# Kernel optimization log

Measured on AMD Instinct MI355X. Metric: run time of the kernel, lower is better.

The kernel has to match this reference:

```python
import jax, jax.numpy as jnp
import numpy as np

# dims: T timesteps (=window_size[0]), B_ = num_windows*batch, window 8x8, C=dim
T, B, WH, WW, C, NH = 4, 1024, 8, 8, 256, 8
HD = C // NH          # head_dim = 32
N = T * WH * WW       # tokens per window volume = 256
V_TH, TAU, ALPHA = 1.0, 2.0, 4.0  # LIF threshold, membrane tau, surrogate sharpness

@jax.custom_vjp
def spike(v):
    # Heaviside spike with sigmoid surrogate gradient (standard spikingjelly-style)
    return (v >= 0.0).astype(v.dtype)

def _spike_fwd(v):
    return spike(v), v

def _spike_bwd(v, g):
    sg = jax.nn.sigmoid(ALPHA * v)
    return (g * ALPHA * sg * (1.0 - sg),)

spike.defvjp(_spike_fwd, _spike_bwd)

def lif(x):
    """Multi-step LIF neuron over leading time axis. x: (T, ...). Hard reset to 0."""
    def step(v, xt):
        v = v + (xt - v) / TAU
        s = spike(v - V_TH)
        return v * (1.0 - s), s
    _, s = jax.lax.scan(step, jnp.zeros_like(x[0]), x)
    return s

def setup_inputs() -> dict:
    key = jax.random.key(0)
    ks = jax.random.split(key, 6)
    sc = 1.0 / np.sqrt(C)
    return {
        "x":   jax.random.normal(ks[0], (T, B, WH, WW, C), jnp.float32),
        "Wq":  jax.random.normal(ks[1], (C, C), jnp.float32) * sc,   # linear_q weight (no bias)
        "Wk":  jax.random.normal(ks[2], (C, C), jnp.float32) * sc,   # linear_k weight (no bias)
        "Wp":  jax.random.normal(ks[3], (C, C), jnp.float32) * sc,   # proj weight
        "bp":  jnp.zeros((C,), jnp.float32),                         # proj bias
        "pos": jax.random.normal(ks[4], (1, NH, N, HD), jnp.float32) * 0.02,  # positional_encoding param
    }

def reference(x, Wq, Wk, Wp, bp, pos):
    # proj_sn on raw input
    xs = lif(x)                                        # (T,B,WH,WW,C) spikes
    # Q path: linear -> spiking neuron (norm=None branch skipped)
    q = lif(xs @ Wq.T)                                 # (T,B,WH,WW,C)
    # K path: linear -> add positional encoding -> spiking neuron
    k = lif(xs @ Wk.T + pos.reshape(T, 1, WH, WW, C))  # (T,B,WH,WW,C)
    # head split exactly as torch reshapes (row-major, mixes T into B for k)
    q = q.reshape(T, B, NH, WH * WW, HD)
    k = k.reshape(B, NH, T * WH * WW, HD)
    # token attention: sum over head_dim, spike, elementwise multiply with k
    att_token = lif(q.sum(-1, keepdims=True))          # (T,B,NH,HW,1)
    attn = k * att_token.reshape(B, NH, -1, 1)         # (B,NH,T*HW,HD)
    # exact torch permute/reshape back to (T,B,WH,WW,C)
    x2 = attn.reshape(B, NH, T, WH, WW, HD).transpose(2, 0, 3, 4, 1, 5).reshape(T, B, WH, WW, C)
    attn_out = lif(x2)                                 # attn_sn output (second return value)
    y = (x2 @ Wp.T + bp).reshape(B, N, C)              # proj then final reshape (B_, N, C)
    return y, attn_out
```

## Files before the change

### kernel.cpp

```cpp
#include <hip/hip_runtime.h>
#include <hip/hip_bf16.h>

static constexpr int  G     = 65536;
static constexpr long PLANE = 16777216L;

__device__ __forceinline__ float bfh(unsigned short u) {
    union { unsigned u32; float f; } c; c.u32 = ((unsigned)u) << 16; return c.f;
}

__global__ void prep_kernel(const float* __restrict__ Wq, const float* __restrict__ Wk,
                            const float* __restrict__ Wp,
                            __hip_bfloat16* __restrict__ WqT, __hip_bfloat16* __restrict__ WkT,
                            float* __restrict__ WpT, unsigned* __restrict__ flag)
{
    int c = blockIdx.x;
    int j = threadIdx.x;
    int idx = c * 256 + j;
    WqT[idx] = __float2bfloat16(Wq[j * 256 + c]);
    WkT[idx] = __float2bfloat16(Wk[j * 256 + c]);
    WpT[idx] = Wp[j * 256 + c];
    if (c == 0 && j == 0) *flag = 0u;
}

__device__ __forceinline__ void gather_word(unsigned long long mm, int j, int lane,
                                            const __hip_bfloat16* __restrict__ WT,
                                            float& q0, float& q1, float& q2, float& q3)
{
    if (!mm) return;
    int b = __ffsll(mm) - 1; mm &= (mm - 1);
    ushort4 w = *((const ushort4*)(WT + (4 * b + j) * 256 + 4 * lane));
    while (mm) {
        int b2 = __ffsll(mm) - 1; mm &= (mm - 1);
        ushort4 w2 = *((const ushort4*)(WT + (4 * b2 + j) * 256 + 4 * lane));
        q0 += bfh(w.x); q1 += bfh(w.y); q2 += bfh(w.z); q3 += bfh(w.w);
        w = w2;
    }
    q0 += bfh(w.x); q1 += bfh(w.y); q2 += bfh(w.z); q3 += bfh(w.w);
}

__device__ __forceinline__ void gather8(
    unsigned long long m0, unsigned long long m1, unsigned long long m2, unsigned long long m3,
    unsigned long long n0, unsigned long long n1, unsigned long long n2, unsigned long long n3,
    const __hip_bfloat16* __restrict__ WT, int lane,
    float4& qa, float4& qb)
{
    const __hip_bfloat16* base = WT + 4 * lane;
    ushort4 w0 = {0,0,0,0}, w1 = {0,0,0,0}, w2 = {0,0,0,0}, w3 = {0,0,0,0};
    ushort4 x0 = {0,0,0,0}, x1 = {0,0,0,0}, x2 = {0,0,0,0}, x3 = {0,0,0,0};
    while (m0 | m1 | m2 | m3 | n0 | n1 | n2 | n3) {
        bool h0 = m0 != 0, h1 = m1 != 0, h2 = m2 != 0, h3 = m3 != 0;
        bool g0 = n0 != 0, g1 = n1 != 0, g2 = n2 != 0, g3 = n3 != 0;
        if (h0) { int b = __ffsll(m0) - 1; m0 &= m0 - 1; w0 = *(const ushort4*)(base + (4*b+0)*256); }
        if (h1) { int b = __ffsll(m1) - 1; m1 &= m1 - 1; w1 = *(const ushort4*)(base + (4*b+1)*256); }
        if (h2) { int b = __ffsll(m2) - 1; m2 &= m2 - 1; w2 = *(const ushort4*)(base + (4*b+2)*256); }
        if (h3) { int b = __ffsll(m3) - 1; m3 &= m3 - 1; w3 = *(const ushort4*)(base + (4*b+3)*256); }
        if (g0) { int b = __ffsll(n0) - 1; n0 &= n0 - 1; x0 = *(const ushort4*)(base + (4*b+0)*256); }
        if (g1) { int b = __ffsll(n1) - 1; n1 &= n1 - 1; x1 = *(const ushort4*)(base + (4*b+1)*256); }
        if (g2) { int b = __ffsll(n2) - 1; n2 &= n2 - 1; x2 = *(const ushort4*)(base + (4*b+2)*256); }
        if (g3) { int b = __ffsll(n3) - 1; n3 &= n3 - 1; x3 = *(const ushort4*)(base + (4*b+3)*256); }
        if (h0) { qa.x += bfh(w0.x); qa.y += bfh(w0.y); qa.z += bfh(w0.z); qa.w += bfh(w0.w); }
        if (h1) { qa.x += bfh(w1.x); qa.y += bfh(w1.y); qa.z += bfh(w1.z); qa.w += bfh(w1.w); }
        if (h2) { qa.x += bfh(w2.x); qa.y += bfh(w2.y); qa.z += bfh(w2.z); qa.w += bfh(w2.w); }
        if (h3) { qa.x += bfh(w3.x); qa.y += bfh(w3.y); qa.z += bfh(w3.z); qa.w += bfh(w3.w); }
        if (g0) { qb.x += bfh(x0.x); qb.y += bfh(x0.y); qb.z += bfh(x0.z); qb.w += bfh(x0.w); }
        if (g1) { qb.x += bfh(x1.x); qb.y += bfh(x1.y); qb.z += bfh(x1.z); qb.w += bfh(x1.w); }
        if (g2) { qb.x += bfh(x2.x); qb.y += bfh(x2.y); qb.z += bfh(x2.z); qb.w += bfh(x2.w); }
        if (g3) { qb.x += bfh(x3.x); qb.y += bfh(x3.y); qb.z += bfh(x3.z); qb.w += bfh(x3.w); }
    }
}

__global__ __launch_bounds__(256) void lif_qk_kernel(
    const float* __restrict__ x,
    unsigned* __restrict__ AM,
    const __hip_bfloat16* __restrict__ WqT,
    const __hip_bfloat16* __restrict__ WkT,
    const float* __restrict__ pos,
    unsigned* __restrict__ flag)
{
    int lane = threadIdx.x & 63;
    int wv   = threadIdx.x >> 6;
    int wid  = blockIdx.x * 4 + wv;
    int sh   = (lane & 56);

    for (int gi = 0; gi < 4; ++gi) {
        int g  = wid * 4 + gi;
        int hw = g & 63;

        float4 X[4];
        #pragma unroll
        for (int t = 0; t < 4; ++t)
            X[t] = ((const float4*)(x + (long)t * PLANE + (long)g * 256))[lane];

        unsigned long long sm[4][4];
        float4 v = make_float4(0.f, 0.f, 0.f, 0.f);
        #pragma unroll
        for (int t = 0; t < 4; ++t) {
            v.x = v.x + (X[t].x - v.x) * 0.5f; bool s0 = (v.x - 1.0f) >= 0.0f; if (s0) v.x = 0.f;
            v.y = v.y + (X[t].y - v.y) * 0.5f; bool s1 = (v.y - 1.0f) >= 0.0f; if (s1) v.y = 0.f;
            v.z = v.z + (X[t].z - v.z) * 0.5f; bool s2 = (v.z - 1.0f) >= 0.0f; if (s2) v.z = 0.f;
            v.w = v.w + (X[t].w - v.w) * 0.5f; bool s3 = (v.w - 1.0f) >= 0.0f; if (s3) v.w = 0.f;
            sm[t][0] = __ballot(s0);
            sm[t][1] = __ballot(s1);
            sm[t][2] = __ballot(s2);
            sm[t][3] = __ballot(s3);
        }

        float4 qs0 = make_float4(0.f,0.f,0.f,0.f), qs1 = make_float4(0.f,0.f,0.f,0.f);
        float4 qs2 = make_float4(0.f,0.f,0.f,0.f), qs3 = make_float4(0.f,0.f,0.f,0.f);
        gather8(sm[0][0], sm[0][1], sm[0][2], sm[0][3],
                sm[1][0], sm[1][1], sm[1][2], sm[1][3], WqT, lane, qs0, qs1);
        gather8(sm[2][0], sm[2][1], sm[2][2], sm[2][3],
                sm[3][0], sm[3][1], sm[3][2], sm[3][3], WqT, lane, qs2, qs3);

        float4 vq = make_float4(0.f, 0.f, 0.f, 0.f);
        float  va = 0.f;
        unsigned attb = 0u;
        #pragma unroll
        for (int t = 0; t < 4; ++t) {
            float4 q = (t == 0) ? qs0 : (t == 1) ? qs1 : (t == 2) ? qs2 : qs3;
            vq.x = vq.x + (q.x - vq.x) * 0.5f; bool t0 = (vq.x - 1.0f) >= 0.0f; if (t0) vq.x = 0.f;
            vq.y = vq.y + (q.y - vq.y) * 0.5f; bool t1 = (vq.y - 1.0f) >= 0.0f; if (t1) vq.y = 0.f;
            vq.z = vq.z + (q.z - vq.z) * 0.5f; bool t2 = (vq.z - 1.0f) >= 0.0f; if (t2) vq.z = 0.f;
            vq.w = vq.w + (q.w - vq.w) * 0.5f; bool t3 = (vq.w - 1.0f) >= 0.0f; if (t3) vq.w = 0.f;
            unsigned long long qb0 = __ballot(t0);
            unsigned long long qb1 = __ballot(t1);
            unsigned long long qb2 = __ballot(t2);
            unsigned long long qb3 = __ballot(t3);

            int cnt = __popc((unsigned)((qb0 >> sh) & 0xFFull))
                    + __popc((unsigned)((qb1 >> sh) & 0xFFull))
                    + __popc((unsigned)((qb2 >> sh) & 0xFFull))
                    + __popc((unsigned)((qb3 >> sh) & 0xFFull));
            va = va + ((float)cnt - va) * 0.5f;
            bool a = (va - 1.0f) >= 0.0f; if (a) va = 0.f;
            attb |= (a ? 1u : 0u) << t;
        }

        bool anyatt = (__ballot(attb != 0u) != 0ull);
        if (!anyatt) {
            if (lane < 32) {
                int t = lane >> 3, wd = lane & 7;
                AM[((long)t * G + g) * 8 + wd] = 0u;
            }
        } else {
            if (lane == 0) atomicOr(flag, 1u);
            float4 vk = make_float4(0.f, 0.f, 0.f, 0.f);
            #pragma unroll
            for (int t = 0; t < 4; ++t) {
                float k0 = 0.f, k1 = 0.f, k2 = 0.f, k3 = 0.f;
                #pragma unroll
                for (int j = 0; j < 4; ++j)
                    gather_word(sm[t][j], j, lane, WkT, k0, k1, k2, k3);
                float4 pp = ((const float4*)(pos + t * 16384 + hw * 256))[lane];
                k0 += pp.x; k1 += pp.y; k2 += pp.z; k3 += pp.w;

                vk.x = vk.x + (k0 - vk.x) * 0.5f; bool t0 = (vk.x - 1.0f) >= 0.0f; if (t0) vk.x = 0.f;
                vk.y = vk.y + (k1 - vk.y) * 0.5f; bool t1 = (vk.y - 1.0f) >= 0.0f; if (t1) vk.y = 0.f;
                vk.z = vk.z + (k2 - vk.z) * 0.5f; bool t2 = (vk.z - 1.0f) >= 0.0f; if (t2) vk.z = 0.f;
                vk.w = vk.w + (k3 - vk.w) * 0.5f; bool t3 = (vk.w - 1.0f) >= 0.0f; if (t3) vk.w = 0.f;

                bool at = ((attb >> t) & 1u) != 0u;
                unsigned long long bb[4];
                bb[0] = __ballot(t0 && at);
                bb[1] = __ballot(t1 && at);
                bb[2] = __ballot(t2 && at);
                bb[3] = __ballot(t3 && at);
                if (lane < 8) {
                    unsigned wdv = 0u;
                    #pragma unroll
                    for (int hd = 0; hd < 32; ++hd) {
                        int ls = lane * 8 + (hd >> 2);
                        wdv |= (unsigned)((bb[hd & 3] >> ls) & 1ull) << hd;
                    }
                    AM[((long)t * G + g) * 8 + lane] = wdv;
                }
            }
        }
    }
}

__global__ __launch_bounds__(256) void out_kernel(
    const unsigned* __restrict__ AM,
    const float* __restrict__ WpT,
    const float* __restrict__ bp,
    const unsigned* __restrict__ flag,
    float* __restrict__ y,
    float* __restrict__ attn_out)
{
    int lane = threadIdx.x & 63;
    int wv   = threadIdx.x >> 6;
    long wave = (long)blockIdx.x * 4 + wv;
    int  nh   = lane >> 3;

    float4 base = ((const float4*)bp)[lane];
    const float4 z = make_float4(0.f, 0.f, 0.f, 0.f);
    long row0 = wave * 32;

    if (*flag == 0u) {
        float4* yp = (float4*)y        + row0 * 64 + lane;
        float4* ap = (float4*)attn_out + row0 * 64 + lane;
        #pragma unroll 8
        for (int r = 0; r < 32; ++r) yp[r * 64] = base;
        #pragma unroll 8
        for (int r = 0; r < 32; ++r) ap[r * 64] = z;
        return;
    }

    int t2  = (int)(row0 >> 16);
    int b2  = (int)(row0 >> 6) & 1023;
    int hw2 = (int)row0 & 63;
    int srow = (b2 * 4 + (nh >> 1)) * 64 + (nh & 1) * 32 + t2 * 8 + (hw2 >> 3);
    unsigned W = AM[(long)srow * 8 + (hw2 & 7)];

    for (int r = 0; r < 32; ++r) {
        long row = row0 + r;
        unsigned Wn = 0u;
        if (r < 31) {
            long rown = row + 1;
            int t2n  = (int)(rown >> 16);
            int b2n  = (int)(rown >> 6) & 1023;
            int hw2n = (int)rown & 63;
            int srn  = (b2n * 4 + (nh >> 1)) * 64 + (nh & 1) * 32 + t2n * 8 + (hw2n >> 3);
            Wn = AM[(long)srn * 8 + (hw2n & 7)];
        }
        float4 val = base;
        if (__ballot(W != 0u) != 0ull) {
            #pragma unroll 1
            for (int n2 = 0; n2 < 8; ++n2) {
                unsigned Wx = __shfl(W, n2 * 8);
                while (Wx) {
                    int hd = __ffs(Wx) - 1;
                    Wx &= (Wx - 1);
                    float4 wl = ((const float4*)(WpT + (n2 * 32 + hd) * 256))[lane];
                    val.x += wl.x; val.y += wl.y; val.z += wl.z; val.w += wl.w;
                }
            }
        }
        ((float4*)y)[row * 64 + lane]        = val;
        ((float4*)attn_out)[row * 64 + lane] = z;
        W = Wn;
    }
}

extern "C" void kernel_launch(void* const* d_in, const int* in_sizes, int n_in,
                              void* d_out, int out_size, void* d_ws, size_t ws_size,
                              hipStream_t stream) {
    const float* x   = (const float*)d_in[0];
    const float* Wq  = (const float*)d_in[1];
    const float* Wk  = (const float*)d_in[2];
    const float* Wp  = (const float*)d_in[3];
    const float* bp  = (const float*)d_in[4];
    const float* pos = (const float*)d_in[5];

    float* y        = (float*)d_out;
    float* attn_out = y + 67108864L;

    char* ws = (char*)d_ws;
    unsigned*           AM   = (unsigned*)(ws);
    __hip_bfloat16*     WqT  = (__hip_bfloat16*)(ws + (8L << 20));
    __hip_bfloat16*     WkT  = (__hip_bfloat16*)(ws + (8L << 20) + (128L << 10));
    float*              WpT  = (float*)(ws + (8L << 20) + (256L << 10));
    unsigned*           flag = (unsigned*)(ws + (8L << 20) + (512L << 10));

    prep_kernel<<<256, 256, 0, stream>>>(Wq, Wk, Wp, WqT, WkT, WpT, flag);
    lif_qk_kernel<<<4096, 256, 0, stream>>>(x, AM, WqT, WkT, pos, flag);
    out_kernel<<<2048, 256, 0, stream>>>(AM, WpT, bp, flag, y, attn_out);
}
```

Before: 791.3 us.

## Compute Q projection with bf16 MFMA on spike matrices instead of sparse gathers

Replaces the per-spike sparse gather-accumulate of Wq rows with dense bf16 MFMA 16x16x32 matrix multiplies. Spike ballots for 16 rows (4 windows x 4 timesteps) are packed into A fragments, and Wq is pre-permuted into an MFMA-friendly fragment layout in the prep kernel. The K path now runs once per wave over four windows and re-reads x to rebuild the spike masks. This removes divergent, data-dependent gather loops, at the cost of doing dense work regardless of spike sparsity and loading x twice when attention fires.

```diff
diff --git a/kernel.cpp b/kernel.cpp
--- a/kernel.cpp
+++ b/kernel.cpp
@@ -4,22 +4,29 @@
 static constexpr int  G     = 65536;
 static constexpr long PLANE = 16777216L;
 
+using bf16x8 = __attribute__((ext_vector_type(8))) short;
+using f32x4  = __attribute__((ext_vector_type(4))) float;
+
 __device__ __forceinline__ float bfh(unsigned short u) {
     union { unsigned u32; float f; } c; c.u32 = ((unsigned)u) << 16; return c.f;
 }
 
 __global__ void prep_kernel(const float* __restrict__ Wq, const float* __restrict__ Wk,
                             const float* __restrict__ Wp,
-                            __hip_bfloat16* __restrict__ WqT, __hip_bfloat16* __restrict__ WkT,
+                            __hip_bfloat16* __restrict__ WqF, __hip_bfloat16* __restrict__ WkT,
                             float* __restrict__ WpT, unsigned* __restrict__ flag)
 {
     int c = blockIdx.x;
     int j = threadIdx.x;
     int idx = c * 256 + j;
-    WqT[idx] = __float2bfloat16(Wq[j * 256 + c]);
     WkT[idx] = __float2bfloat16(Wk[j * 256 + c]);
     WpT[idx] = Wp[j * 256 + c];
-    if (c == 0 && j == 0) *flag = 0u;
+    int jj = idx & 7, cc = (idx >> 3) & 15, hi = (idx >> 7) & 3,
+        ntile = (idx >> 9) & 15, chunk = (idx >> 13) & 7;
+    int n = ntile * 16 + cc;
+    int k = chunk * 32 + hi * 8 + jj;
+    WqF[idx] = __float2bfloat16(Wq[n * 256 + k]);
+    if (idx == 0) *flag = 0u;
 }
 
 __device__ __forceinline__ void gather_word(unsigned long long mm, int j, int lane,
@@ -38,112 +45,129 @@
     q0 += bfh(w.x); q1 += bfh(w.y); q2 += bfh(w.z); q3 += bfh(w.w);
 }
 
-__device__ __forceinline__ void gather8(
-    unsigned long long m0, unsigned long long m1, unsigned long long m2, unsigned long long m3,
-    unsigned long long n0, unsigned long long n1, unsigned long long n2, unsigned long long n3,
-    const __hip_bfloat16* __restrict__ WT, int lane,
-    float4& qa, float4& qb)
-{
-    const __hip_bfloat16* base = WT + 4 * lane;
-    ushort4 w0 = {0,0,0,0}, w1 = {0,0,0,0}, w2 = {0,0,0,0}, w3 = {0,0,0,0};
-    ushort4 x0 = {0,0,0,0}, x1 = {0,0,0,0}, x2 = {0,0,0,0}, x3 = {0,0,0,0};
-    while (m0 | m1 | m2 | m3 | n0 | n1 | n2 | n3) {
-        bool h0 = m0 != 0, h1 = m1 != 0, h2 = m2 != 0, h3 = m3 != 0;
-        bool g0 = n0 != 0, g1 = n1 != 0, g2 = n2 != 0, g3 = n3 != 0;
-        if (h0) { int b = __ffsll(m0) - 1; m0 &= m0 - 1; w0 = *(const ushort4*)(base + (4*b+0)*256); }
-        if (h1) { int b = __ffsll(m1) - 1; m1 &= m1 - 1; w1 = *(const ushort4*)(base + (4*b+1)*256); }
-        if (h2) { int b = __ffsll(m2) - 1; m2 &= m2 - 1; w2 = *(const ushort4*)(base + (4*b+2)*256); }
-        if (h3) { int b = __ffsll(m3) - 1; m3 &= m3 - 1; w3 = *(const ushort4*)(base + (4*b+3)*256); }
-        if (g0) { int b = __ffsll(n0) - 1; n0 &= n0 - 1; x0 = *(const ushort4*)(base + (4*b+0)*256); }
-        if (g1) { int b = __ffsll(n1) - 1; n1 &= n1 - 1; x1 = *(const ushort4*)(base + (4*b+1)*256); }
-        if (g2) { int b = __ffsll(n2) - 1; n2 &= n2 - 1; x2 = *(const ushort4*)(base + (4*b+2)*256); }
-        if (g3) { int b = __ffsll(n3) - 1; n3 &= n3 - 1; x3 = *(const ushort4*)(base + (4*b+3)*256); }
-        if (h0) { qa.x += bfh(w0.x); qa.y += bfh(w0.y); qa.z += bfh(w0.z); qa.w += bfh(w0.w); }
-        if (h1) { qa.x += bfh(w1.x); qa.y += bfh(w1.y); qa.z += bfh(w1.z); qa.w += bfh(w1.w); }
-        if (h2) { qa.x += bfh(w2.x); qa.y += bfh(w2.y); qa.z += bfh(w2.z); qa.w += bfh(w2.w); }
-        if (h3) { qa.x += bfh(w3.x); qa.y += bfh(w3.y); qa.z += bfh(w3.z); qa.w += bfh(w3.w); }
-        if (g0) { qb.x += bfh(x0.x); qb.y += bfh(x0.y); qb.z += bfh(x0.z); qb.w += bfh(x0.w); }
-        if (g1) { qb.x += bfh(x1.x); qb.y += bfh(x1.y); qb.z += bfh(x1.z); qb.w += bfh(x1.w); }
-        if (g2) { qb.x += bfh(x2.x); qb.y += bfh(x2.y); qb.z += bfh(x2.z); qb.w += bfh(x2.w); }
-        if (g3) { qb.x += bfh(x3.x); qb.y += bfh(x3.y); qb.z += bfh(x3.z); qb.w += bfh(x3.w); }
-    }
-}
-
 __global__ __launch_bounds__(256) void lif_qk_kernel(
     const float* __restrict__ x,
     unsigned* __restrict__ AM,
-    const __hip_bfloat16* __restrict__ WqT,
+    const __hip_bfloat16* __restrict__ WqF,
     const __hip_bfloat16* __restrict__ WkT,
     const float* __restrict__ pos,
     unsigned* __restrict__ flag)
 {
-    int lane = threadIdx.x & 63;
-    int wv   = threadIdx.x >> 6;
-    int wid  = blockIdx.x * 4 + wv;
-    int sh   = (lane & 56);
-
-    for (int gi = 0; gi < 4; ++gi) {
-        int g  = wid * 4 + gi;
-        int hw = g & 63;
-
-        float4 X[4];
-        #pragma unroll
-        for (int t = 0; t < 4; ++t)
-            X[t] = ((const float4*)(x + (long)t * PLANE + (long)g * 256))[lane];
-
-        unsigned long long sm[4][4];
+    int lane  = threadIdx.x & 63;
+    int wv    = threadIdx.x >> 6;
+    int wid   = blockIdx.x * 4 + wv;
+    int hi    = lane >> 4;
+    int myrow = lane & 15;
+    int tksh  = lane & 48;
+
+    unsigned long long mm0 = 0, mm1 = 0, mm2 = 0, mm3 = 0;
+    #pragma unroll
+    for (int tk = 0; tk < 4; ++tk) {
+        int g = wid * 4 + tk;
+        float4 X0 = ((const float4*)(x + 0L * PLANE + (long)g * 256))[lane];
+        float4 X1 = ((const float4*)(x + 1L * PLANE + (long)g * 256))[lane];
+        float4 X2 = ((const float4*)(x + 2L * PLANE + (long)g * 256))[lane];
+        float4 X3 = ((const float4*)(x + 3L * PLANE + (long)g * 256))[lane];
         float4 v = make_float4(0.f, 0.f, 0.f, 0.f);
         #pragma unroll
         for (int t = 0; t < 4; ++t) {
-            v.x = v.x + (X[t].x - v.x) * 0.5f; bool s0 = (v.x - 1.0f) >= 0.0f; if (s0) v.x = 0.f;
-            v.y = v.y + (X[t].y - v.y) * 0.5f; bool s1 = (v.y - 1.0f) >= 0.0f; if (s1) v.y = 0.f;
-            v.z = v.z + (X[t].z - v.z) * 0.5f; bool s2 = (v.z - 1.0f) >= 0.0f; if (s2) v.z = 0.f;
-            v.w = v.w + (X[t].w - v.w) * 0.5f; bool s3 = (v.w - 1.0f) >= 0.0f; if (s3) v.w = 0.f;
-            sm[t][0] = __ballot(s0);
-            sm[t][1] = __ballot(s1);
-            sm[t][2] = __ballot(s2);
-            sm[t][3] = __ballot(s3);
-        }
-
-        float4 qs0 = make_float4(0.f,0.f,0.f,0.f), qs1 = make_float4(0.f,0.f,0.f,0.f);
-        float4 qs2 = make_float4(0.f,0.f,0.f,0.f), qs3 = make_float4(0.f,0.f,0.f,0.f);
-        gather8(sm[0][0], sm[0][1], sm[0][2], sm[0][3],
-                sm[1][0], sm[1][1], sm[1][2], sm[1][3], WqT, lane, qs0, qs1);
-        gather8(sm[2][0], sm[2][1], sm[2][2], sm[2][3],
-                sm[3][0], sm[3][1], sm[3][2], sm[3][3], WqT, lane, qs2, qs3);
-
-        float4 vq = make_float4(0.f, 0.f, 0.f, 0.f);
-        float  va = 0.f;
-        unsigned attb = 0u;
+            float4 X = (t == 0) ? X0 : (t == 1) ? X1 : (t == 2) ? X2 : X3;
+            v.x = v.x + (X.x - v.x) * 0.5f; bool s0 = (v.x - 1.0f) >= 0.0f; if (s0) v.x = 0.f;
+            v.y = v.y + (X.y - v.y) * 0.5f; bool s1 = (v.y - 1.0f) >= 0.0f; if (s1) v.y = 0.f;
+            v.z = v.z + (X.z - v.z) * 0.5f; bool s2 = (v.z - 1.0f) >= 0.0f; if (s2) v.z = 0.f;
+            v.w = v.w + (X.w - v.w) * 0.5f; bool s3 = (v.w - 1.0f) >= 0.0f; if (s3) v.w = 0.f;
+            unsigned long long b0 = __ballot(s0);
+            unsigned long long b1 = __ballot(s1);
+            unsigned long long b2 = __ballot(s2);
+            unsigned long long b3 = __ballot(s3);
+            bool sel = (myrow == tk * 4 + t);
+            if (sel) { mm0 = b0; mm1 = b1; mm2 = b2; mm3 = b3; }
+        }
+    }
+
+    bf16x8 af[8];
+    #pragma unroll
+    for (int ch = 0; ch < 8; ++ch) {
+        int bb = ch * 8 + hi * 2;
+        unsigned w0 = (unsigned)(mm0 >> bb);
+        unsigned w1 = (unsigned)(mm1 >> bb);
+        unsigned w2 = (unsigned)(mm2 >> bb);
+        unsigned w3 = (unsigned)(mm3 >> bb);
+        bf16x8 a;
+        a[0] = (w0 & 1u) ? (short)0x3F80 : (short)0;
+        a[1] = (w1 & 1u) ? (short)0x3F80 : (short)0;
+        a[2] = (w2 & 1u) ? (short)0x3F80 : (short)0;
+        a[3] = (w3 & 1u) ? (short)0x3F80 : (short)0;
+        a[4] = ((w0 >> 1) & 1u) ? (short)0x3F80 : (short)0;
+        a[5] = ((w1 >> 1) & 1u) ? (short)0x3F80 : (short)0;
+        a[6] = ((w2 >> 1) & 1u) ? (short)0x3F80 : (short)0;
+        a[7] = ((w3 >> 1) & 1u) ? (short)0x3F80 : (short)0;
+        af[ch] = a;
+    }
+
+    const char* wqf = (const char*)WqF;
+    unsigned attw = 0u;
+    for (int h = 0; h < 8; ++h) {
+        unsigned long long bal[2][4];
+        #pragma unroll
+        for (int sub = 0; sub < 2; ++sub) {
+            int nt = h * 2 + sub;
+            f32x4 acc = {0.f, 0.f, 0.f, 0.f};
+            #pragma unroll
+            for (int ch = 0; ch < 8; ++ch) {
+                bf16x8 b = *(const bf16x8*)(wqf + (ch << 14) + (nt << 10) + (lane << 4));
+                acc = __builtin_amdgcn_mfma_f32_16x16x32_bf16(af[ch], b, acc, 0, 0, 0);
+            }
+            float vq = 0.f;
+            #pragma unroll
+            for (int t = 0; t < 4; ++t) {
+                vq = vq + (acc[t] - vq) * 0.5f;
+                bool sp = (vq - 1.0f) >= 0.0f; if (sp) vq = 0.f;
+                bal[sub][t] = __ballot(sp);
+            }
+        }
+        float va = 0.f;
         #pragma unroll
         for (int t = 0; t < 4; ++t) {
-            float4 q = (t == 0) ? qs0 : (t == 1) ? qs1 : (t == 2) ? qs2 : qs3;
-            vq.x = vq.x + (q.x - vq.x) * 0.5f; bool t0 = (vq.x - 1.0f) >= 0.0f; if (t0) vq.x = 0.f;
-            vq.y = vq.y + (q.y - vq.y) * 0.5f; bool t1 = (vq.y - 1.0f) >= 0.0f; if (t1) vq.y = 0.f;
-            vq.z = vq.z + (q.z - vq.z) * 0.5f; bool t2 = (vq.z - 1.0f) >= 0.0f; if (t2) vq.z = 0.f;
-            vq.w = vq.w + (q.w - vq.w) * 0.5f; bool t3 = (vq.w - 1.0f) >= 0.0f; if (t3) vq.w = 0.f;
-            unsigned long long qb0 = __ballot(t0);
-            unsigned long long qb1 = __ballot(t1);
-            unsigned long long qb2 = __ballot(t2);
-            unsigned long long qb3 = __ballot(t3);
-
-            int cnt = __popc((unsigned)((qb0 >> sh) & 0xFFull))
-                    + __popc((unsigned)((qb1 >> sh) & 0xFFull))
-                    + __popc((unsigned)((qb2 >> sh) & 0xFFull))
-                    + __popc((unsigned)((qb3 >> sh) & 0xFFull));
+            int cnt = __popc((unsigned)(bal[0][t] >> tksh) & 0xFFFFu)
+                    + __popc((unsigned)(bal[1][t] >> tksh) & 0xFFFFu);
             va = va + ((float)cnt - va) * 0.5f;
             bool a = (va - 1.0f) >= 0.0f; if (a) va = 0.f;
-            attb |= (a ? 1u : 0u) << t;
-        }
-
-        bool anyatt = (__ballot(attb != 0u) != 0ull);
-        if (!anyatt) {
-            if (lane < 32) {
-                int t = lane >> 3, wd = lane & 7;
-                AM[((long)t * G + g) * 8 + wd] = 0u;
-            }
-        } else {
-            if (lane == 0) atomicOr(flag, 1u);
+            attw |= (a ? 1u : 0u) << (h * 4 + t);
+        }
+    }
+
+    bool anyatt = (__ballot(attw != 0u) != 0ull);
+    if (!anyatt) {
+        if (lane < 32) {
+            int t = lane >> 3, wd = lane & 7;
+            #pragma unroll
+            for (int tk = 0; tk < 4; ++tk)
+                AM[((long)t * G + (wid * 4 + tk)) * 8 + wd] = 0u;
+        }
+    } else {
+        if (lane == 0) atomicOr(flag, 1u);
+        for (int tk = 0; tk < 4; ++tk) {
+            int g  = wid * 4 + tk;
+            int hw = g & 63;
+            unsigned attw_tk = __shfl(attw, tk * 16);
+            unsigned long long sm[4][4];
+            {
+                float4 v = make_float4(0.f, 0.f, 0.f, 0.f);
+                #pragma unroll
+                for (int t = 0; t < 4; ++t) {
+                    float4 X = ((const float4*)(x + (long)t * PLANE + (long)g * 256))[lane];
+                    v.x = v.x + (X.x - v.x) * 0.5f; bool s0 = (v.x - 1.0f) >= 0.0f; if (s0) v.x = 0.f;
+                    v.y = v.y + (X.y - v.y) * 0.5f; bool s1 = (v.y - 1.0f) >= 0.0f; if (s1) v.y = 0.f;
+                    v.z = v.z + (X.z - v.z) * 0.5f; bool s2 = (v.z - 1.0f) >= 0.0f; if (s2) v.z = 0.f;
+                    v.w = v.w + (X.w - v.w) * 0.5f; bool s3 = (v.w - 1.0f) >= 0.0f; if (s3) v.w = 0.f;
+                    sm[t][0] = __ballot(s0);
+                    sm[t][1] = __ballot(s1);
+                    sm[t][2] = __ballot(s2);
+                    sm[t][3] = __ballot(s3);
+                }
+            }
+            unsigned attb = (attw_tk >> ((lane >> 3) * 4)) & 0xFu;
             float4 vk = make_float4(0.f, 0.f, 0.f, 0.f);
             #pragma unroll
             for (int t = 0; t < 4; ++t) {
@@ -257,12 +281,12 @@
 
     char* ws = (char*)d_ws;
     unsigned*           AM   = (unsigned*)(ws);
-    __hip_bfloat16*     WqT  = (__hip_bfloat16*)(ws + (8L << 20));
+    __hip_bfloat16*     WqF  = (__hip_bfloat16*)(ws + (8L << 20));
     __hip_bfloat16*     WkT  = (__hip_bfloat16*)(ws + (8L << 20) + (128L << 10));
     float*              WpT  = (float*)(ws + (8L << 20) + (256L << 10));
     unsigned*           flag = (unsigned*)(ws + (8L << 20) + (512L << 10));
 
-    prep_kernel<<<256, 256, 0, stream>>>(Wq, Wk, Wp, WqT, WkT, WpT, flag);
-    lif_qk_kernel<<<4096, 256, 0, stream>>>(x, AM, WqT, WkT, pos, flag);
+    prep_kernel<<<256, 256, 0, stream>>>(Wq, Wk, Wp, WqF, WkT, WpT, flag);
+    lif_qk_kernel<<<4096, 256, 0, stream>>>(x, AM, WqF, WkT, pos, flag);
     out_kernel<<<2048, 256, 0, stream>>>(AM, WpT, bp, flag, y, attn_out);
 }
```

Result: slower. 815.9 us (+3.1%).
